# Performance work log

Measured on AMD Instinct MI355X. Metric: run time of the kernel, lower is better.

## Reference

```python
import jax, jax.numpy as jnp
import numpy as np

B, T, C, U = 256, 512, 512, 512  # batch, timesteps, n_in, units


def setup_inputs() -> dict:
    key = jax.random.key(0)
    k1, k2, k3, k4 = jax.random.split(key, 4)
    x = jax.random.normal(k1, (B, T, C), dtype=jnp.float32)
    dones = (jax.random.uniform(k2, (B, T, 1)) < 0.05).astype(jnp.float32)
    # keras 'uniform' initializer default range is [-0.05, 0.05]
    wx = jax.random.uniform(k3, (C, 4 * U), jnp.float32, -0.05, 0.05)
    wh = jax.random.uniform(k4, (U, 4 * U), jnp.float32, -0.05, 0.05)
    b = jnp.zeros((4 * U,), jnp.float32)
    return {"x": x, "dones": dones, "wx": wx, "wh": wh, "b": b}


def reference(x, dones, wx, wh, b):
    # x: [B,T,C], dones: [B,T,1], wx: [C,4U], wh: [U,4U], b: [4U]
    Bn, Tn, Cn = x.shape
    Un = wh.shape[0]

    def step(carry, xt):
        c, h = carry                     # [B,U] each
        xi, dt = xt                      # xi: [B,C], dt: [B,1]
        keep = 1.0 - dt
        c = c * keep
        h = h * keep
        z = xi @ wx + h @ wh + b         # [B,4U]
        i, f, o, u = jnp.split(z, 4, axis=-1)
        i = jax.nn.sigmoid(i)
        f = jax.nn.sigmoid(f)
        o = jax.nn.sigmoid(o)
        u = jnp.tanh(u)
        c = f * c + i * u
        h = o * jnp.tanh(c)
        return (c, h), h

    c0 = jnp.zeros((Bn, Un), x.dtype)   # self.states starts at zeros
    h0 = jnp.zeros((Bn, Un), x.dtype)
    (c, h), hs = jax.lax.scan(step, (c0, h0), (x.transpose(1, 0, 2), dones.transpose(1, 0, 2)))
    xs = hs.transpose(1, 0, 2)          # [B,T,U] (return_sequence=True)
    s = jnp.concatenate([c, h], axis=-1)  # [B,2U] (squeezed final state)
    return xs, s
```

## Files before the change

kernel.cpp:

```cpp
#include <hip/hip_runtime.h>

#define BATCH 256
#define TT 512
#define CIN 512
#define UU 512
#define ZN 2048
#define BT (BATCH*TT)

typedef __attribute__((ext_vector_type(8))) short short8;
typedef __attribute__((ext_vector_type(4))) float f32x4;
typedef __attribute__((ext_vector_type(4))) unsigned u32x4;

__device__ __forceinline__ short f2bf(float f){
  unsigned u = __float_as_uint(f);
  u += 0x7fffu + ((u >> 16) & 1u);
  return (short)(u >> 16);
}
__device__ __forceinline__ float bf2f(unsigned short s){
  unsigned u = ((unsigned)s) << 16;
  return __uint_as_float(u);
}

#define GLD16(g, l) __builtin_amdgcn_global_load_lds( \
    (const __attribute__((address_space(1))) void*)(g), \
    (__attribute__((address_space(3))) void*)(l), 16, 0, 0)

#define CLOAD(dst, p, OFFSTR) asm volatile( \
    "global_load_dwordx4 %0, %1, off offset:" OFFSTR " sc0 sc1" \
    : "=v"(dst) : "v"(p) : "memory")

__device__ __forceinline__ void st_coh_u32(void* p, unsigned v){
  asm volatile("global_store_dword %0, %1, off sc0 sc1" :: "v"(p), "v"(v) : "memory");
}

__device__ __forceinline__ float sigm(float x){ return 1.0f/(1.0f + __expf(-x)); }
__device__ __forceinline__ float tanh_fast(float x){ return 1.0f - 2.0f/(1.0f + __expf(2.0f*x)); }

__global__ __launch_bounds__(256) void convert_x_kernel(const float* __restrict__ x,
                                                        short* __restrict__ xb){
  const long total = (long)TT*BATCH*64;
  const long stride = (long)gridDim.x * blockDim.x;
  for (long i = (long)blockIdx.x * blockDim.x + threadIdx.x; i < total; i += stride){
    const int c8 = (int)(i & 63);
    const long tb = i >> 6;
    const int b = (int)(tb & (BATCH-1));
    const int t = (int)(tb >> 8);
    const float* src = x + ((long)b*TT + t)*CIN + c8*8;
    const float4 v0 = *(const float4*)(src);
    const float4 v1 = *(const float4*)(src + 4);
    short8 o;
    o[0]=f2bf(v0.x); o[1]=f2bf(v0.y); o[2]=f2bf(v0.z); o[3]=f2bf(v0.w);
    o[4]=f2bf(v1.x); o[5]=f2bf(v1.y); o[6]=f2bf(v1.z); o[7]=f2bf(v1.w);
    *(short8*)(xb + i*8) = o;
  }
}

__global__ __launch_bounds__(256) void transpose_w_kernel(
    const float* __restrict__ wx, const float* __restrict__ wh,
    short* __restrict__ wxt, short* __restrict__ wht){
  const float* src = blockIdx.z ? wh : wx;
  short* dst = blockIdx.z ? wht : wxt;
  __shared__ float tile[32][33];
  const int nt = blockIdx.x << 5;
  const int kt = blockIdx.y << 5;
  const int tx = threadIdx.x & 31, ty = threadIdx.x >> 5;
  #pragma unroll
  for (int i = 0; i < 32; i += 8)
    tile[ty+i][tx] = src[(long)(kt+ty+i)*ZN + nt+tx];
  __syncthreads();
  #pragma unroll
  for (int i = 0; i < 32; i += 8)
    dst[(long)(nt+ty+i)*512 + kt+tx] = f2bf(tile[tx][ty+i]);
}

__global__ __launch_bounds__(256) void gemm_xpart_kernel(
    const short* __restrict__ A, const short* __restrict__ Bt,
    const float* __restrict__ bias, short* __restrict__ Co){
  __shared__ short As[128*32];
  __shared__ short Bs[128*32];
  const int wg = blockIdx.x;
  const int xcd = wg & 7;
  const int ii = wg >> 3;
  const long m0 = (long)(xcd*128 + (ii >> 4)) << 7;
  const long n0 = (long)(ii & 15) << 7;
  const int tid = threadIdx.x;
  const int lane = tid & 63;
  const int wave = tid >> 6;
  const int wm = wave & 1, wn = wave >> 1;
  f32x4 acc[4][4] = {};
  const int srow = tid >> 2;
  const int sseg = tid & 3;
  const long aoff = (m0 + srow) * 512 + sseg * 8;
  const long boff = (n0 + srow) * 512 + sseg * 8;
  short* ldsa = &As[tid * 8];
  short* ldsb = &Bs[tid * 8];
  for (int k0 = 0; k0 < 512; k0 += 32){
    __syncthreads();
    GLD16(A + aoff + k0, ldsa);
    GLD16(A + aoff + 64*512 + k0, ldsa + 2048);
    GLD16(Bt + boff + k0, ldsb);
    GLD16(Bt + boff + 64*512 + k0, ldsb + 2048);
    __syncthreads();
    const int kb = (lane >> 4) * 8;
    short8 af[4], bf[4];
    #pragma unroll
    for (int mi = 0; mi < 4; mi++) af[mi] = *(const short8*)&As[(wm*64 + mi*16 + (lane&15))*32 + kb];
    #pragma unroll
    for (int ni = 0; ni < 4; ni++) bf[ni] = *(const short8*)&Bs[(wn*64 + ni*16 + (lane&15))*32 + kb];
    #pragma unroll
    for (int mi = 0; mi < 4; mi++)
      #pragma unroll
      for (int ni = 0; ni < 4; ni++)
        acc[mi][ni] = __builtin_amdgcn_mfma_f32_16x16x32_bf16(af[mi], bf[ni], acc[mi][ni], 0, 0, 0);
  }
  #pragma unroll
  for (int ni = 0; ni < 4; ni++){
    const long col = n0 + wn*64 + ni*16 + (lane & 15);
    const float bv = bias[col];
    #pragma unroll
    for (int mi = 0; mi < 4; mi++){
      const long row = m0 + wm*64 + mi*16 + ((lane >> 4) << 2);
      #pragma unroll
      for (int r = 0; r < 4; r++)
        Co[(row + r)*ZN + col] = f2bf(acc[mi][ni][r] + bv);
    }
  }
}

__global__ __launch_bounds__(512, 1) void lstm_persist_kernel(
    const short* __restrict__ xpart, const float* __restrict__ dones,
    const short* __restrict__ wht, unsigned* __restrict__ ht0,
    unsigned* __restrict__ ht1, float* __restrict__ out){
  __shared__ short h_lds[8192];
  __shared__ float zpart[128*19 + 16];
  const int tid = threadIdx.x;
  const int lane = tid & 63;
  const int wv = tid >> 6;
  const int bg = blockIdx.x & 15;
  const int cg = blockIdx.x >> 4;
  const int rb = bg << 4;
  const int uc = cg << 5;
  const int j = lane & 15;
  const int hq = lane >> 4;
  const int g_w = wv >> 1;
  const int ucl = ((wv & 1) << 4) + j;
  const int zl = g_w*32 + ucl;

  short8 bfr[16];
  {
    const short* wsrc = wht + ((long)(g_w*512 + uc + ucl))*512 + hq*8;
    #pragma unroll
    for (int m = 0; m < 16; m++)
      bfr[m] = *(const short8*)(wsrc + m*32);
  }

  const int srow = tid & 15;
  const int skg  = tid >> 4;
  const long hoff = (long)(rb + srow)*UU + skg*16;
  short* sdst = h_lds + skg*256 + srow*8;

  const int erow = tid >> 5;
  const int euj  = tid & 31;
  const int eucol = uc + euj;
  const int row  = rb + erow;

  const unsigned short* xp16 = (const unsigned short*)xpart;

  float c = 0.0f;
  float dn;
  unsigned short xp[4];
  dn = dones[(long)row*TT];
  #pragma unroll
  for (int g = 0; g < 4; g++)
    xp[g] = xp16[(long)row*ZN + (g<<9) + eucol];

  for (int t = 0; t < TT; t++){
    {
      const unsigned* hs = ((t & 1) ? ht1 : ht0) + hoff;
      const unsigned tg = (unsigned)t;
      u32x4 w0, w1, w2, w3;
      for (;;){
        CLOAD(w0, hs, "0"); CLOAD(w1, hs, "16");
        CLOAD(w2, hs, "32"); CLOAD(w3, hs, "48");
        asm volatile("s_waitcnt vmcnt(0)" ::: "memory");
        const unsigned d = (w0[0]^tg)|(w0[1]^tg)|(w0[2]^tg)|(w0[3]^tg)
                         | (w1[0]^tg)|(w1[1]^tg)|(w1[2]^tg)|(w1[3]^tg)
                         | (w2[0]^tg)|(w2[1]^tg)|(w2[2]^tg)|(w2[3]^tg)
                         | (w3[0]^tg)|(w3[1]^tg)|(w3[2]^tg)|(w3[3]^tg);
        if (__all((int)((d & 0xffffu) == 0u))) break;
        __builtin_amdgcn_s_sleep(1);
      }
      u32x4 pa, pb;
      pa[0] = (w0[0]>>16) | (w0[1] & 0xffff0000u);
      pa[1] = (w0[2]>>16) | (w0[3] & 0xffff0000u);
      pa[2] = (w1[0]>>16) | (w1[1] & 0xffff0000u);
      pa[3] = (w1[2]>>16) | (w1[3] & 0xffff0000u);
      pb[0] = (w2[0]>>16) | (w2[1] & 0xffff0000u);
      pb[1] = (w2[2]>>16) | (w2[3] & 0xffff0000u);
      pb[2] = (w3[0]>>16) | (w3[1] & 0xffff0000u);
      pb[3] = (w3[2]>>16) | (w3[3] & 0xffff0000u);
      *(u32x4*)(sdst)       = pa;
      *(u32x4*)(sdst + 128) = pb;
    }
    __syncthreads();
    const short* abase = h_lds + lane*8;
    f32x4 acc0 = {}, acc1 = {};
    #pragma unroll
    for (int m = 0; m < 16; m += 2){
      const short8 a0 = *(const short8*)(abase + m*512);
      const short8 a1 = *(const short8*)(abase + m*512 + 512);
      acc0 = __builtin_amdgcn_mfma_f32_16x16x32_bf16(a0, bfr[m],   acc0, 0, 0, 0);
      acc1 = __builtin_amdgcn_mfma_f32_16x16x32_bf16(a1, bfr[m+1], acc1, 0, 0, 0);
    }
    const f32x4 acc = acc0 + acc1;
    #pragma unroll
    for (int r = 0; r < 4; r++)
      zpart[zl*19 + hq*4 + r] = acc[r];
    __syncthreads();
    const float keep = 1.0f - dn;
    const float cold = c * keep;
    const float z0 = bf2f(xp[0]) + keep*zpart[(0*32 + euj)*19 + erow];
    const float z1 = bf2f(xp[1]) + keep*zpart[(1*32 + euj)*19 + erow];
    const float z2 = bf2f(xp[2]) + keep*zpart[(2*32 + euj)*19 + erow];
    const float z3 = bf2f(xp[3]) + keep*zpart[(3*32 + euj)*19 + erow];
    const float gi = sigm(z0);
    const float gf = sigm(z1);
    const float go = sigm(z2);
    const float gu = tanh_fast(z3);
    const float cn = gf*cold + gi*gu;
    const float hn = go * tanh_fast(cn);
    c = cn;
    if (t == TT-1){
      out[(long)row*TT*UU + (long)t*UU + eucol] = hn;
      float* s = out + (long)BATCH*TT*UU;
      s[(long)row*2*UU + eucol] = cn;
      s[(long)row*2*UU + UU + eucol] = hn;
    } else {
      unsigned* hd = (t & 1) ? ht0 : ht1;
      const unsigned hv = ((unsigned)(unsigned short)f2bf(hn) << 16) | (unsigned)(t+1);
      st_coh_u32(hd + (long)row*UU + eucol, hv);
      out[(long)row*TT*UU + (long)t*UU + eucol] = hn;
      dn = dones[(long)row*TT + (t+1)];
      const long xb = ((long)(t+1)*BATCH + row)*ZN + eucol;
      #pragma unroll
      for (int g = 0; g < 4; g++)
        xp[g] = xp16[xb + (g<<9)];
    }
  }
}

extern "C" void kernel_launch(void* const* d_in, const int* in_sizes, int n_in,
                              void* d_out, int out_size, void* d_ws, size_t ws_size,
                              hipStream_t stream){
  const float* x     = (const float*)d_in[0];
  const float* dones = (const float*)d_in[1];
  const float* wx    = (const float*)d_in[2];
  const float* wh    = (const float*)d_in[3];
  const float* b     = (const float*)d_in[4];
  float* out = (float*)d_out;
  char* ws = (char*)d_ws;
  short* x_tb  = (short*)(ws);
  short* wx_t  = (short*)(ws + 134217728L);
  short* wh_t  = (short*)(ws + 136314880L);
  short* xpart = (short*)(ws + 138412032L);
  unsigned* ht0 = (unsigned*)(ws + 675282944L);
  unsigned* ht1 = (unsigned*)(ws + 675807232L);

  hipMemsetAsync(ht0, 0, 524288, stream);
  hipMemsetAsync(ht1, 0, 524288, stream);
  convert_x_kernel<<<2048, 256, 0, stream>>>(x, x_tb);
  transpose_w_kernel<<<dim3(64,16,2), 256, 0, stream>>>(wx, wh, wx_t, wh_t);
  gemm_xpart_kernel<<<16384, 256, 0, stream>>>(x_tb, wx_t, b, xpart);
  lstm_persist_kernel<<<256, 512, 0, stream>>>(xpart, dones, wh_t, ht0, ht1, out);
}
```

Before: 1.755 ms.

## Fuse input projection GEMM into persistent LSTM recurrence kernel

Removes the separate x-to-bf16 conversion and the large input-projection GEMM, so the persistent recurrent kernel now computes x@Wx on the fly with both Wx and Wh fragments kept in registers. It double-buffers the h and x tiles in LDS and restructures the gate layout so each wave does the cross-gate exchange through a small per-wave LDS buffer without a second block barrier. This avoids writing and re-reading a large bf16 pre-activation tensor and two extra launches. In exchange, each serial timestep does twice the MFMA work and carries higher register pressure, which could lengthen the critical path.

```diff
diff --git a/kernel.cpp b/kernel.cpp
--- a/kernel.cpp
+++ b/kernel.cpp
@@ -5,7 +5,6 @@
 #define CIN 512
 #define UU 512
 #define ZN 2048
-#define BT (BATCH*TT)
 
 typedef __attribute__((ext_vector_type(8))) short short8;
 typedef __attribute__((ext_vector_type(4))) float f32x4;
@@ -16,14 +15,6 @@
   u += 0x7fffu + ((u >> 16) & 1u);
   return (short)(u >> 16);
 }
-__device__ __forceinline__ float bf2f(unsigned short s){
-  unsigned u = ((unsigned)s) << 16;
-  return __uint_as_float(u);
-}
-
-#define GLD16(g, l) __builtin_amdgcn_global_load_lds( \
-    (const __attribute__((address_space(1))) void*)(g), \
-    (__attribute__((address_space(3))) void*)(l), 16, 0, 0)
 
 #define CLOAD(dst, p, OFFSTR) asm volatile( \
     "global_load_dwordx4 %0, %1, off offset:" OFFSTR " sc0 sc1" \
@@ -35,25 +26,6 @@
 
 __device__ __forceinline__ float sigm(float x){ return 1.0f/(1.0f + __expf(-x)); }
 __device__ __forceinline__ float tanh_fast(float x){ return 1.0f - 2.0f/(1.0f + __expf(2.0f*x)); }
-
-__global__ __launch_bounds__(256) void convert_x_kernel(const float* __restrict__ x,
-                                                        short* __restrict__ xb){
-  const long total = (long)TT*BATCH*64;
-  const long stride = (long)gridDim.x * blockDim.x;
-  for (long i = (long)blockIdx.x * blockDim.x + threadIdx.x; i < total; i += stride){
-    const int c8 = (int)(i & 63);
-    const long tb = i >> 6;
-    const int b = (int)(tb & (BATCH-1));
-    const int t = (int)(tb >> 8);
-    const float* src = x + ((long)b*TT + t)*CIN + c8*8;
-    const float4 v0 = *(const float4*)(src);
-    const float4 v1 = *(const float4*)(src + 4);
-    short8 o;
-    o[0]=f2bf(v0.x); o[1]=f2bf(v0.y); o[2]=f2bf(v0.z); o[3]=f2bf(v0.w);
-    o[4]=f2bf(v1.x); o[5]=f2bf(v1.y); o[6]=f2bf(v1.z); o[7]=f2bf(v1.w);
-    *(short8*)(xb + i*8) = o;
-  }
-}
 
 __global__ __launch_bounds__(256) void transpose_w_kernel(
     const float* __restrict__ wx, const float* __restrict__ wh,
@@ -73,110 +45,78 @@
     dst[(long)(nt+ty+i)*512 + kt+tx] = f2bf(tile[tx][ty+i]);
 }
 
-__global__ __launch_bounds__(256) void gemm_xpart_kernel(
-    const short* __restrict__ A, const short* __restrict__ Bt,
-    const float* __restrict__ bias, short* __restrict__ Co){
-  __shared__ short As[128*32];
-  __shared__ short Bs[128*32];
-  const int wg = blockIdx.x;
-  const int xcd = wg & 7;
-  const int ii = wg >> 3;
-  const long m0 = (long)(xcd*128 + (ii >> 4)) << 7;
-  const long n0 = (long)(ii & 15) << 7;
+__global__ __launch_bounds__(512, 1) void lstm_fused_kernel(
+    const float* __restrict__ x, const float* __restrict__ dones,
+    const short* __restrict__ wht, const short* __restrict__ wxt,
+    const float* __restrict__ bias, unsigned* __restrict__ ht0,
+    unsigned* __restrict__ ht1, float* __restrict__ out){
+  __shared__ short h_lds[2][8192];
+  __shared__ short x_lds[2][8192];
+  __shared__ float zw[2048];
   const int tid = threadIdx.x;
-  const int lane = tid & 63;
-  const int wave = tid >> 6;
-  const int wm = wave & 1, wn = wave >> 1;
-  f32x4 acc[4][4] = {};
-  const int srow = tid >> 2;
-  const int sseg = tid & 3;
-  const long aoff = (m0 + srow) * 512 + sseg * 8;
-  const long boff = (n0 + srow) * 512 + sseg * 8;
-  short* ldsa = &As[tid * 8];
-  short* ldsb = &Bs[tid * 8];
-  for (int k0 = 0; k0 < 512; k0 += 32){
-    __syncthreads();
-    GLD16(A + aoff + k0, ldsa);
-    GLD16(A + aoff + 64*512 + k0, ldsa + 2048);
-    GLD16(Bt + boff + k0, ldsb);
-    GLD16(Bt + boff + 64*512 + k0, ldsb + 2048);
-    __syncthreads();
-    const int kb = (lane >> 4) * 8;
-    short8 af[4], bf[4];
-    #pragma unroll
-    for (int mi = 0; mi < 4; mi++) af[mi] = *(const short8*)&As[(wm*64 + mi*16 + (lane&15))*32 + kb];
-    #pragma unroll
-    for (int ni = 0; ni < 4; ni++) bf[ni] = *(const short8*)&Bs[(wn*64 + ni*16 + (lane&15))*32 + kb];
-    #pragma unroll
-    for (int mi = 0; mi < 4; mi++)
-      #pragma unroll
-      for (int ni = 0; ni < 4; ni++)
-        acc[mi][ni] = __builtin_amdgcn_mfma_f32_16x16x32_bf16(af[mi], bf[ni], acc[mi][ni], 0, 0, 0);
-  }
-  #pragma unroll
-  for (int ni = 0; ni < 4; ni++){
-    const long col = n0 + wn*64 + ni*16 + (lane & 15);
-    const float bv = bias[col];
-    #pragma unroll
-    for (int mi = 0; mi < 4; mi++){
-      const long row = m0 + wm*64 + mi*16 + ((lane >> 4) << 2);
-      #pragma unroll
-      for (int r = 0; r < 4; r++)
-        Co[(row + r)*ZN + col] = f2bf(acc[mi][ni][r] + bv);
-    }
-  }
-}
-
-__global__ __launch_bounds__(512, 1) void lstm_persist_kernel(
-    const short* __restrict__ xpart, const float* __restrict__ dones,
-    const short* __restrict__ wht, unsigned* __restrict__ ht0,
-    unsigned* __restrict__ ht1, float* __restrict__ out){
-  __shared__ short h_lds[8192];
-  __shared__ float zpart[128*19 + 16];
-  const int tid = threadIdx.x;
-  const int lane = tid & 63;
+  const int l = tid & 63;
   const int wv = tid >> 6;
   const int bg = blockIdx.x & 15;
   const int cg = blockIdx.x >> 4;
   const int rb = bg << 4;
   const int uc = cg << 5;
-  const int j = lane & 15;
-  const int hq = lane >> 4;
-  const int g_w = wv >> 1;
-  const int ucl = ((wv & 1) << 4) + j;
-  const int zl = g_w*32 + ucl;
-
-  short8 bfr[16];
+  const int hq = l >> 4;
+  const int g_l = l & 3;
+  const int u_l = (l >> 2) & 3;
+  const int s_l = l & 3;
+
+  short8 bh[16], bx[16];
+  const long zcol = (long)(g_l*512 + uc + wv*4 + u_l);
   {
-    const short* wsrc = wht + ((long)(g_w*512 + uc + ucl))*512 + hq*8;
+    const short* whs = wht + zcol*512 + hq*8;
+    const short* wxs = wxt + zcol*512 + hq*8;
     #pragma unroll
-    for (int m = 0; m < 16; m++)
-      bfr[m] = *(const short8*)(wsrc + m*32);
+    for (int m = 0; m < 16; m++){
+      bh[m] = *(const short8*)(whs + m*32);
+      bx[m] = *(const short8*)(wxs + m*32);
+    }
   }
+  const float bias_l = bias[zcol];
 
   const int srow = tid & 15;
   const int skg  = tid >> 4;
   const long hoff = (long)(rb + srow)*UU + skg*16;
-  short* sdst = h_lds + skg*256 + srow*8;
-
-  const int erow = tid >> 5;
-  const int euj  = tid & 31;
-  const int eucol = uc + euj;
-  const int row  = rb + erow;
-
-  const unsigned short* xp16 = (const unsigned short*)xpart;
+  const int sdst = skg*256 + srow*8;
+  const float* xsrc = x + ((long)(rb + srow)*TT)*CIN + skg*16;
+
+  const int crow = rb + hq*4 + s_l;
+  const int cucol = uc + wv*4 + u_l;
+  unsigned* const hst0 = ht0 + (long)crow*UU + cucol;
+  unsigned* const hst1 = ht1 + (long)crow*UU + cucol;
 
   float c = 0.0f;
-  float dn;
-  unsigned short xp[4];
-  dn = dones[(long)row*TT];
-  #pragma unroll
-  for (int g = 0; g < 4; g++)
-    xp[g] = xp16[(long)row*ZN + (g<<9) + eucol];
+  float dn0, dn1, dn2, dn3, dn_c;
+  {
+    const long db = (long)(rb + hq*4)*TT;
+    dn0 = dones[db];
+    dn1 = dones[db + TT];
+    dn2 = dones[db + 2*TT];
+    dn3 = dones[db + 3*TT];
+    dn_c = dones[(long)crow*TT];
+  }
+  float4 xr0 = *(const float4*)(xsrc);
+  float4 xr1 = *(const float4*)(xsrc + 4);
+  float4 xr2 = *(const float4*)(xsrc + 8);
+  float4 xr3 = *(const float4*)(xsrc + 12);
 
   for (int t = 0; t < TT; t++){
+    const int p = t & 1;
     {
-      const unsigned* hs = ((t & 1) ? ht1 : ht0) + hoff;
+      short8 xv0, xv1;
+      xv0[0]=f2bf(xr0.x); xv0[1]=f2bf(xr0.y); xv0[2]=f2bf(xr0.z); xv0[3]=f2bf(xr0.w);
+      xv0[4]=f2bf(xr1.x); xv0[5]=f2bf(xr1.y); xv0[6]=f2bf(xr1.z); xv0[7]=f2bf(xr1.w);
+      xv1[0]=f2bf(xr2.x); xv1[1]=f2bf(xr2.y); xv1[2]=f2bf(xr2.z); xv1[3]=f2bf(xr2.w);
+      xv1[4]=f2bf(xr3.x); xv1[5]=f2bf(xr3.y); xv1[6]=f2bf(xr3.z); xv1[7]=f2bf(xr3.w);
+      *(short8*)&x_lds[p][sdst      ] = xv0;
+      *(short8*)&x_lds[p][sdst + 128] = xv1;
+    }
+    {
+      const unsigned* hs = (p ? ht1 : ht0) + hoff;
       const unsigned tg = (unsigned)t;
       u32x4 w0, w1, w2, w3;
       for (;;){
@@ -199,52 +139,58 @@
       pb[1] = (w2[2]>>16) | (w2[3] & 0xffff0000u);
       pb[2] = (w3[0]>>16) | (w3[1] & 0xffff0000u);
       pb[3] = (w3[2]>>16) | (w3[3] & 0xffff0000u);
-      *(u32x4*)(sdst)       = pa;
-      *(u32x4*)(sdst + 128) = pb;
+      *(u32x4*)&h_lds[p][sdst      ] = pa;
+      *(u32x4*)&h_lds[p][sdst + 128] = pb;
     }
     __syncthreads();
-    const short* abase = h_lds + lane*8;
-    f32x4 acc0 = {}, acc1 = {};
+    const short* ah = &h_lds[p][l*8];
+    const short* ax = &x_lds[p][l*8];
+    f32x4 h0 = {}, h1 = {}, x0 = {}, x1 = {};
     #pragma unroll
     for (int m = 0; m < 16; m += 2){
-      const short8 a0 = *(const short8*)(abase + m*512);
-      const short8 a1 = *(const short8*)(abase + m*512 + 512);
-      acc0 = __builtin_amdgcn_mfma_f32_16x16x32_bf16(a0, bfr[m],   acc0, 0, 0, 0);
-      acc1 = __builtin_amdgcn_mfma_f32_16x16x32_bf16(a1, bfr[m+1], acc1, 0, 0, 0);
-    }
-    const f32x4 acc = acc0 + acc1;
-    #pragma unroll
-    for (int r = 0; r < 4; r++)
-      zpart[zl*19 + hq*4 + r] = acc[r];
-    __syncthreads();
-    const float keep = 1.0f - dn;
-    const float cold = c * keep;
-    const float z0 = bf2f(xp[0]) + keep*zpart[(0*32 + euj)*19 + erow];
-    const float z1 = bf2f(xp[1]) + keep*zpart[(1*32 + euj)*19 + erow];
-    const float z2 = bf2f(xp[2]) + keep*zpart[(2*32 + euj)*19 + erow];
-    const float z3 = bf2f(xp[3]) + keep*zpart[(3*32 + euj)*19 + erow];
+      h0 = __builtin_amdgcn_mfma_f32_16x16x32_bf16(*(const short8*)(ah + m*512),       bh[m],   h0, 0, 0, 0);
+      x0 = __builtin_amdgcn_mfma_f32_16x16x32_bf16(*(const short8*)(ax + m*512),       bx[m],   x0, 0, 0, 0);
+      h1 = __builtin_amdgcn_mfma_f32_16x16x32_bf16(*(const short8*)(ah + m*512 + 512), bh[m+1], h1, 0, 0, 0);
+      x1 = __builtin_amdgcn_mfma_f32_16x16x32_bf16(*(const short8*)(ax + m*512 + 512), bx[m+1], x1, 0, 0, 0);
+    }
+    f32x4 zfull;
+    zfull[0] = (x0[0] + x1[0] + bias_l) + (1.0f - dn0)*(h0[0] + h1[0]);
+    zfull[1] = (x0[1] + x1[1] + bias_l) + (1.0f - dn1)*(h0[1] + h1[1]);
+    zfull[2] = (x0[2] + x1[2] + bias_l) + (1.0f - dn2)*(h0[2] + h1[2]);
+    zfull[3] = (x0[3] + x1[3] + bias_l) + (1.0f - dn3)*(h0[3] + h1[3]);
+    *(f32x4*)&zw[wv*256 + l*4] = zfull;
+    const int rbw = wv*256 + (hq*16 + u_l*4)*4 + s_l;
+    const float z0 = zw[rbw];
+    const float z1 = zw[rbw + 4];
+    const float z2 = zw[rbw + 8];
+    const float z3 = zw[rbw + 12];
+    const float keep = 1.0f - dn_c;
     const float gi = sigm(z0);
     const float gf = sigm(z1);
     const float go = sigm(z2);
     const float gu = tanh_fast(z3);
-    const float cn = gf*cold + gi*gu;
+    const float cn = gf*(c*keep) + gi*gu;
     const float hn = go * tanh_fast(cn);
     c = cn;
+    out[(long)crow*TT*UU + (long)t*UU + cucol] = hn;
     if (t == TT-1){
-      out[(long)row*TT*UU + (long)t*UU + eucol] = hn;
       float* s = out + (long)BATCH*TT*UU;
-      s[(long)row*2*UU + eucol] = cn;
-      s[(long)row*2*UU + UU + eucol] = hn;
+      s[(long)crow*2*UU + cucol] = cn;
+      s[(long)crow*2*UU + UU + cucol] = hn;
     } else {
-      unsigned* hd = (t & 1) ? ht0 : ht1;
       const unsigned hv = ((unsigned)(unsigned short)f2bf(hn) << 16) | (unsigned)(t+1);
-      st_coh_u32(hd + (long)row*UU + eucol, hv);
-      out[(long)row*TT*UU + (long)t*UU + eucol] = hn;
-      dn = dones[(long)row*TT + (t+1)];
-      const long xb = ((long)(t+1)*BATCH + row)*ZN + eucol;
-      #pragma unroll
-      for (int g = 0; g < 4; g++)
-        xp[g] = xp16[xb + (g<<9)];
+      st_coh_u32(p ? hst0 : hst1, hv);
+      const float* xs = xsrc + (long)(t+1)*CIN;
+      xr0 = *(const float4*)(xs);
+      xr1 = *(const float4*)(xs + 4);
+      xr2 = *(const float4*)(xs + 8);
+      xr3 = *(const float4*)(xs + 12);
+      const long db = (long)(rb + hq*4)*TT + (t+1);
+      dn0 = dones[db];
+      dn1 = dones[db + TT];
+      dn2 = dones[db + 2*TT];
+      dn3 = dones[db + 3*TT];
+      dn_c = dones[(long)crow*TT + (t+1)];
     }
   }
 }
@@ -259,17 +205,13 @@
   const float* b     = (const float*)d_in[4];
   float* out = (float*)d_out;
   char* ws = (char*)d_ws;
-  short* x_tb  = (short*)(ws);
-  short* wx_t  = (short*)(ws + 134217728L);
-  short* wh_t  = (short*)(ws + 136314880L);
-  short* xpart = (short*)(ws + 138412032L);
-  unsigned* ht0 = (unsigned*)(ws + 675282944L);
-  unsigned* ht1 = (unsigned*)(ws + 675807232L);
+  short* wx_t  = (short*)(ws);
+  short* wh_t  = (short*)(ws + 2097152L);
+  unsigned* ht0 = (unsigned*)(ws + 4194304L);
+  unsigned* ht1 = (unsigned*)(ws + 4718592L);
 
   hipMemsetAsync(ht0, 0, 524288, stream);
   hipMemsetAsync(ht1, 0, 524288, stream);
-  convert_x_kernel<<<2048, 256, 0, stream>>>(x, x_tb);
   transpose_w_kernel<<<dim3(64,16,2), 256, 0, stream>>>(wx, wh, wx_t, wh_t);
-  gemm_xpart_kernel<<<16384, 256, 0, stream>>>(x_tb, wx_t, b, xpart);
-  lstm_persist_kernel<<<256, 512, 0, stream>>>(xpart, dones, wh_t, ht0, ht1, out);
-}
+  lstm_fused_kernel<<<256, 512, 0, stream>>>(x, dones, wh_t, wx_t, b, ht0, ht1, out);
+}
```

Result: slower. 2.851 ms (+62.5%).

## Remap LSTM gate columns per wave to drop second block barrier; add poll hint

Applied to the files above, without the earlier changes.

Reassigns MFMA output columns so each wave computes all four gates for its own units, which lets the gate exchange happen through a per-wave LDS region without the second __syncthreads. The LDS h buffer is double-buffered by timestep parity so the next step's writes cannot race readers of the previous step. A cheap single-dword poll is added before the full 64-byte coherent poll to cut memory traffic while spinning. The cost is extra per-step loads of the dones flags (five instead of one) and a changed thread-to-output mapping that affects store coalescing.

```diff
diff --git a/kernel.cpp b/kernel.cpp
--- a/kernel.cpp
+++ b/kernel.cpp
@@ -27,6 +27,9 @@
 
 #define CLOAD(dst, p, OFFSTR) asm volatile( \
     "global_load_dwordx4 %0, %1, off offset:" OFFSTR " sc0 sc1" \
+    : "=v"(dst) : "v"(p) : "memory")
+#define CLOADW(dst, p) asm volatile( \
+    "global_load_dword %0, %1, off sc0 sc1" \
     : "=v"(dst) : "v"(p) : "memory")
 
 __device__ __forceinline__ void st_coh_u32(void* p, unsigned v){
@@ -131,24 +134,23 @@
     const short* __restrict__ xpart, const float* __restrict__ dones,
     const short* __restrict__ wht, unsigned* __restrict__ ht0,
     unsigned* __restrict__ ht1, float* __restrict__ out){
-  __shared__ short h_lds[8192];
-  __shared__ float zpart[128*19 + 16];
+  __shared__ short h_lds[2][8192];
+  __shared__ float zw[2048];
   const int tid = threadIdx.x;
-  const int lane = tid & 63;
+  const int l = tid & 63;
   const int wv = tid >> 6;
   const int bg = blockIdx.x & 15;
   const int cg = blockIdx.x >> 4;
   const int rb = bg << 4;
   const int uc = cg << 5;
-  const int j = lane & 15;
-  const int hq = lane >> 4;
-  const int g_w = wv >> 1;
-  const int ucl = ((wv & 1) << 4) + j;
-  const int zl = g_w*32 + ucl;
+  const int hq = l >> 4;
+  const int g_l = l & 3;
+  const int u_l = (l >> 2) & 3;
+  const int s_l = l & 3;
 
   short8 bfr[16];
   {
-    const short* wsrc = wht + ((long)(g_w*512 + uc + ucl))*512 + hq*8;
+    const short* wsrc = wht + ((long)(g_l*512 + uc + wv*4 + u_l))*512 + hq*8;
     #pragma unroll
     for (int m = 0; m < 16; m++)
       bfr[m] = *(const short8*)(wsrc + m*32);
@@ -157,27 +159,39 @@
   const int srow = tid & 15;
   const int skg  = tid >> 4;
   const long hoff = (long)(rb + srow)*UU + skg*16;
-  short* sdst = h_lds + skg*256 + srow*8;
-
-  const int erow = tid >> 5;
-  const int euj  = tid & 31;
-  const int eucol = uc + euj;
-  const int row  = rb + erow;
-
+  const int sdst = skg*256 + srow*8;
+
+  const int crow = rb + hq*4 + s_l;
+  const int cucol = uc + wv*4 + u_l;
   const unsigned short* xp16 = (const unsigned short*)xpart;
 
   float c = 0.0f;
-  float dn;
+  float dn0, dn1, dn2, dn3, dn_c;
+  {
+    const long db = (long)(rb + hq*4)*TT;
+    dn0 = dones[db];
+    dn1 = dones[db + TT];
+    dn2 = dones[db + 2*TT];
+    dn3 = dones[db + 3*TT];
+    dn_c = dones[(long)crow*TT];
+  }
   unsigned short xp[4];
-  dn = dones[(long)row*TT];
   #pragma unroll
   for (int g = 0; g < 4; g++)
-    xp[g] = xp16[(long)row*ZN + (g<<9) + eucol];
+    xp[g] = xp16[(long)crow*ZN + (g<<9) + cucol];
 
   for (int t = 0; t < TT; t++){
+    const int p = t & 1;
     {
-      const unsigned* hs = ((t & 1) ? ht1 : ht0) + hoff;
+      const unsigned* hs = (p ? ht1 : ht0) + hoff;
       const unsigned tg = (unsigned)t;
+      unsigned hint;
+      for (;;){
+        CLOADW(hint, hs);
+        asm volatile("s_waitcnt vmcnt(0)" ::: "memory");
+        if (__all((int)((hint & 0xffffu) == tg))) break;
+        __builtin_amdgcn_s_sleep(1);
+      }
       u32x4 w0, w1, w2, w3;
       for (;;){
         CLOAD(w0, hs, "0"); CLOAD(w1, hs, "16");
@@ -199,49 +213,57 @@
       pb[1] = (w2[2]>>16) | (w2[3] & 0xffff0000u);
       pb[2] = (w3[0]>>16) | (w3[1] & 0xffff0000u);
       pb[3] = (w3[2]>>16) | (w3[3] & 0xffff0000u);
-      *(u32x4*)(sdst)       = pa;
-      *(u32x4*)(sdst + 128) = pb;
+      *(u32x4*)&h_lds[p][sdst      ] = pa;
+      *(u32x4*)&h_lds[p][sdst + 128] = pb;
     }
     __syncthreads();
-    const short* abase = h_lds + lane*8;
-    f32x4 acc0 = {}, acc1 = {};
+    const short* ah = &h_lds[p][l*8];
+    f32x4 a0 = {}, a1 = {};
     #pragma unroll
     for (int m = 0; m < 16; m += 2){
-      const short8 a0 = *(const short8*)(abase + m*512);
-      const short8 a1 = *(const short8*)(abase + m*512 + 512);
-      acc0 = __builtin_amdgcn_mfma_f32_16x16x32_bf16(a0, bfr[m],   acc0, 0, 0, 0);
-      acc1 = __builtin_amdgcn_mfma_f32_16x16x32_bf16(a1, bfr[m+1], acc1, 0, 0, 0);
-    }
-    const f32x4 acc = acc0 + acc1;
-    #pragma unroll
-    for (int r = 0; r < 4; r++)
-      zpart[zl*19 + hq*4 + r] = acc[r];
-    __syncthreads();
-    const float keep = 1.0f - dn;
-    const float cold = c * keep;
-    const float z0 = bf2f(xp[0]) + keep*zpart[(0*32 + euj)*19 + erow];
-    const float z1 = bf2f(xp[1]) + keep*zpart[(1*32 + euj)*19 + erow];
-    const float z2 = bf2f(xp[2]) + keep*zpart[(2*32 + euj)*19 + erow];
-    const float z3 = bf2f(xp[3]) + keep*zpart[(3*32 + euj)*19 + erow];
+      a0 = __builtin_amdgcn_mfma_f32_16x16x32_bf16(*(const short8*)(ah + m*512),       bfr[m],   a0, 0, 0, 0);
+      a1 = __builtin_amdgcn_mfma_f32_16x16x32_bf16(*(const short8*)(ah + m*512 + 512), bfr[m+1], a1, 0, 0, 0);
+    }
+    f32x4 zf;
+    zf[0] = (1.0f - dn0)*(a0[0] + a1[0]);
+    zf[1] = (1.0f - dn1)*(a0[1] + a1[1]);
+    zf[2] = (1.0f - dn2)*(a0[2] + a1[2]);
+    zf[3] = (1.0f - dn3)*(a0[3] + a1[3]);
+    *(f32x4*)&zw[wv*256 + l*4] = zf;
+    const int rbw = wv*256 + (hq*16 + u_l*4)*4 + s_l;
+    const float zh0 = zw[rbw];
+    const float zh1 = zw[rbw + 4];
+    const float zh2 = zw[rbw + 8];
+    const float zh3 = zw[rbw + 12];
+    const float keep = 1.0f - dn_c;
+    const float z0 = bf2f(xp[0]) + zh0;
+    const float z1 = bf2f(xp[1]) + zh1;
+    const float z2 = bf2f(xp[2]) + zh2;
+    const float z3 = bf2f(xp[3]) + zh3;
     const float gi = sigm(z0);
     const float gf = sigm(z1);
     const float go = sigm(z2);
     const float gu = tanh_fast(z3);
-    const float cn = gf*cold + gi*gu;
+    const float cn = gf*(c*keep) + gi*gu;
     const float hn = go * tanh_fast(cn);
     c = cn;
     if (t == TT-1){
-      out[(long)row*TT*UU + (long)t*UU + eucol] = hn;
+      out[(long)crow*TT*UU + (long)t*UU + cucol] = hn;
       float* s = out + (long)BATCH*TT*UU;
-      s[(long)row*2*UU + eucol] = cn;
-      s[(long)row*2*UU + UU + eucol] = hn;
+      s[(long)crow*2*UU + cucol] = cn;
+      s[(long)crow*2*UU + UU + cucol] = hn;
     } else {
-      unsigned* hd = (t & 1) ? ht0 : ht1;
+      unsigned* hd = (p ? ht0 : ht1);
       const unsigned hv = ((unsigned)(unsigned short)f2bf(hn) << 16) | (unsigned)(t+1);
-      st_coh_u32(hd + (long)row*UU + eucol, hv);
-      out[(long)row*TT*UU + (long)t*UU + eucol] = hn;
-      dn = dones[(long)row*TT + (t+1)];
-      const long xb = ((long)(t+1)*BATCH + row)*ZN + eucol;
+      st_coh_u32(hd + (long)crow*UU + cucol, hv);
+      out[(long)crow*TT*UU + (long)t*UU + cucol] = hn;
+      const long db = (long)(rb + hq*4)*TT + (t+1);
+      dn0 = dones[db];
+      dn1 = dones[db + TT];
+      dn2 = dones[db + 2*TT];
+      dn3 = dones[db + 3*TT];
+      dn_c = dones[(long)crow*TT + (t+1)];
+      const long xb = ((long)(t+1)*BATCH + crow)*ZN + cucol;
       #pragma unroll
       for (int g = 0; g < 4; g++)
         xp[g] = xp16[xb + (g<<9)];
```

Measured after the change: 3.108 ms. +77.1%, slower.
